# Kernel optimization log

Hardware: AMD Instinct MI355X
Metric: run time of the kernel (lower is better)

Reference implementation:

```python
import jax, jax.numpy as jnp
import numpy as np

N_QUBITS = 10
DEPTH = 5
DIM = 2 ** N_QUBITS  # 1024
NUM_CLASSES = 2
BATCH = 16384
IN_DIM = 784


def _rot_matrices(w):
    # w: [depth, n_qubits, 3] angles (phi, theta, omega); qml.Rot = RZ(omega) RY(theta) RZ(phi)
    phi, theta, omega = w[..., 0], w[..., 1], w[..., 2]
    c, s = jnp.cos(theta / 2), jnp.sin(theta / 2)
    e = lambda a: jnp.exp(1j * a.astype(jnp.complex64))
    m00 = e(-(phi + omega) / 2) * c
    m01 = -e((phi - omega) / 2) * s
    m10 = e(-(phi - omega) / 2) * s
    m11 = e((phi + omega) / 2) * c
    return jnp.stack([jnp.stack([m00, m01], -1), jnp.stack([m10, m11], -1)], -2)  # [D, n, 2, 2]


def _apply_1q(state, U, w):
    # state: [B] + [2]*n ; apply 2x2 U on qubit axis w
    s = jnp.moveaxis(state, w + 1, -1)
    s = s @ U.T
    return jnp.moveaxis(s, -1, w + 1)


def _apply_cnot(state, c, t):
    s = jnp.moveaxis(state, (c + 1, t + 1), (-2, -1))
    s = jnp.concatenate([s[..., 0:1, :], s[..., 1:2, ::-1]], axis=-2)  # flip target where control=1
    return jnp.moveaxis(s, (-2, -1), (c + 1, t + 1))


def _circuit(x, weights):
    B = x.shape[0]
    # AmplitudeEmbedding: pad_with=0, normalize=True
    amp = jnp.pad(x, ((0, 0), (0, DIM - x.shape[1])))
    amp = amp / jnp.linalg.norm(amp, axis=1, keepdims=True)
    state = amp.astype(jnp.complex64).reshape((B,) + (2,) * N_QUBITS)
    U = _rot_matrices(weights)
    for d in range(DEPTH):
        for i in range(N_QUBITS):  # entangling CNOT ring
            state = _apply_cnot(state, i, (i + 1) % N_QUBITS)
        for i in range(N_QUBITS):  # per-qubit Rot
            state = _apply_1q(state, U[d, i], i)
    probs = (state.real ** 2 + state.imag ** 2).reshape(B, DIM)
    # <Z_i> = P(bit_i = 0) - P(bit_i = 1)
    z = []
    for i in range(N_QUBITS):
        p = probs.reshape(B, 2 ** i, 2, -1)
        z.append(p[:, :, 0, :].sum((1, 2)) - p[:, :, 1, :].sum((1, 2)))
    return jnp.stack(z, axis=1)  # [B, n_qubits]


def setup_inputs() -> dict:
    key = jax.random.key(0)
    k1, k2, k3 = jax.random.split(key, 3)
    x = jax.random.normal(k1, (BATCH, IN_DIM), dtype=jnp.float32)
    weights = jax.random.uniform(k2, (DEPTH, N_QUBITS, 3), dtype=jnp.float32) * (2.0 * np.pi)
    y = jax.random.randint(k3, (BATCH,), 0, NUM_CLASSES)
    return {"x": x, "weights": weights, "y": y}


def reference(x, weights, y):
    logits = _circuit(x, weights)[:, :NUM_CLASSES]
    logp = jax.nn.log_softmax(logits, axis=-1)
    loss = -jnp.take_along_axis(logp, y[:, None], axis=1).mean()
    return loss
```

## Files before the change

### kernel.cpp

```cpp
#include <hip/hip_runtime.h>
#include <type_traits>

#define NQ 10
#define N_DEPTH 5
#define DIM 1024
#define BATCH 16384
#define IN_DIM 784
#define NGATES 50
#define KPAD 800
#define KALLOC 832
#define NT 13
#define NSLOT 768
#define NB 6

typedef float f32x2 __attribute__((ext_vector_type(2)));
typedef float f32x4 __attribute__((ext_vector_type(4)));
typedef short bf16x8 __attribute__((ext_vector_type(8)));
typedef unsigned u32x4 __attribute__((ext_vector_type(4)));

struct MaskTab {
  unsigned v[NGATES];
  unsigned p[NGATES];
  unsigned vz0, vz1;
};

constexpr MaskTab make_masks() {
  MaskTab t{};
  unsigned v[NQ], p[NQ];
  for (int i = 0; i < NQ; ++i) { v[i] = 1u << (9 - i); p[i] = 1u << (9 - i); }
  for (int d = 0; d < N_DEPTH; ++d) {
    for (int i = 0; i < NQ; ++i) {
      int c = i, tt = (i + 1) % NQ;
      v[tt] ^= v[c];
      p[c]  ^= p[tt];
    }
    for (int i = 0; i < NQ; ++i) {
      t.v[d * NQ + i] = v[i];
      t.p[d * NQ + i] = p[i];
    }
  }
  t.vz0 = v[0];
  t.vz1 = v[1];
  return t;
}

constexpr MaskTab MT = make_masks();
__constant__ MaskTab d_MT = make_masks();

struct PermTab { short slot[DIM]; };
constexpr PermTab make_perm() {
  PermTab t{};
  int a = 0, b = 256, c = 512;
  for (int m = 0; m < DIM; ++m) {
    const int p0 = __builtin_popcount((unsigned)m & MT.vz0) & 1;
    const int p1 = __builtin_popcount((unsigned)m & MT.vz1) & 1;
    if (p0 && !p1)      t.slot[m] = (short)a++;
    else if (!p0 && p1) t.slot[m] = (short)b++;
    else if (p0 && p1)  t.slot[m] = (short)c++;
    else                t.slot[m] = -1;
  }
  return t;
}
__constant__ PermTab d_PT = make_perm();

__device__ __forceinline__ f32x2 ampfma(f32x2 o, f32x2 q, f32x2 co, f32x2 cp) {
  f32x2 d;
  asm("v_pk_mul_f32 %0, %2, %1 op_sel:[0,0] op_sel_hi:[0,1]\n\t"
      "v_pk_fma_f32 %0, %2, %1, %0 op_sel:[1,1,0] op_sel_hi:[1,0,1] neg_lo:[1,0,0]\n\t"
      "v_pk_fma_f32 %0, %3, %4, %0 op_sel:[0,0,0] op_sel_hi:[0,1,1]\n\t"
      "v_pk_fma_f32 %0, %3, %4, %0 op_sel:[1,1,0] op_sel_hi:[1,0,1] neg_lo:[1,0,0]"
      : "=&v"(d)
      : "v"(o), "v"(co), "v"(cp), "v"(q));
  return d;
}

__device__ __forceinline__ float fxor(float x, unsigned m) {
  return __uint_as_float(__float_as_uint(x) ^ m);
}

__device__ __forceinline__ unsigned bf16pack(float lo, float hi) {
  unsigned a = __float_as_uint(lo), b = __float_as_uint(hi);
  unsigned ra = (a + 0x7fffu + ((a >> 16) & 1u)) >> 16;
  unsigned rb = (b + 0x7fffu + ((b >> 16) & 1u)) >> 16;
  return (ra & 0xffffu) | (rb << 16);
}

__device__ __forceinline__ unsigned cvtpk(float a, float b) {
  unsigned d;
  asm("v_cvt_pk_bf16_f32 %0, %1, %2" : "=v"(d) : "v"(a), "v"(b));
  return d;
}

__device__ __forceinline__ void gll16(const void* g, void* l) {
  __builtin_amdgcn_global_load_lds(
      (const __attribute__((address_space(1))) void*)g,
      (__attribute__((address_space(3))) void*)l, 16, 0, 0);
}

__global__ __launch_bounds__(256) void prep(const float* __restrict__ X,
                                            unsigned* __restrict__ Xb,
                                            float* __restrict__ xn2,
                                            const float* __restrict__ w,
                                            unsigned* __restrict__ W2u) {
  __shared__ f32x4 UL4[NGATES];
  __shared__ f32x2 S0[DIM];
  __shared__ f32x2 S1[DIM];

  const int tid = threadIdx.x;

  if (blockIdx.x >= 832) {
    const int row = (blockIdx.x - 832) * 8 + (tid >> 5);
    const int l32 = tid & 31;
    const float* src = X + (size_t)row * IN_DIM;
    unsigned* dst = Xb + (size_t)row * (KPAD / 2);
    float ssq = 0.0f;
    for (int c = l32; c < 100; c += 32) {
      u32x4 out;
      if (c < 98) {
        f32x4 v0 = *(const f32x4*)(src + c * 8);
        f32x4 v1 = *(const f32x4*)(src + c * 8 + 4);
        ssq += v0.x * v0.x + v0.y * v0.y + v0.z * v0.z + v0.w * v0.w +
               v1.x * v1.x + v1.y * v1.y + v1.z * v1.z + v1.w * v1.w;
        out = u32x4{cvtpk(v0.x, v0.y), cvtpk(v0.z, v0.w),
                    cvtpk(v1.x, v1.y), cvtpk(v1.z, v1.w)};
      } else {
        out = u32x4{0, 0, 0, 0};
      }
      *(u32x4*)(dst + c * 4) = out;
    }
#pragma unroll
    for (int off = 1; off < 32; off <<= 1) ssq += __shfl_xor(ssq, off);
    if (l32 == 0) xn2[row] = ssq;
    return;
  }

  if (tid < NGATES) {
    float phi = w[tid * 3 + 0], th = w[tid * 3 + 1], om = w[tid * 3 + 2];
    float ct = cosf(th * 0.5f), st = sinf(th * 0.5f);
    float aa = (phi + om) * 0.5f, bb = (phi - om) * 0.5f;
    float cA = cosf(aa), sA = sinf(aa), cB = cosf(bb), sB = sinf(bb);
    UL4[tid] = f32x4{ ct * cA, -ct * sA, -st * cB, -st * sB };
  }

  const int j = blockIdx.x;
  unsigned* rowp = W2u + (size_t)j * NSLOT;

  if (j >= IN_DIM) {
#pragma unroll
    for (int k = 0; k < 3; ++k) rowp[tid + k * 256] = 0u;
    return;
  }

#pragma unroll
  for (int k = 0; k < 4; ++k) {
    const int m = tid + k * 256;
    S0[m] = f32x2{(m == j) ? 1.0f : 0.0f, 0.0f};
  }
  __syncthreads();

  for (int g = 0; g < NGATES; ++g) {
    const f32x2* src = (g & 1) ? S1 : S0;
    f32x2* dst = (g & 1) ? S0 : S1;
    const f32x4 A = UL4[g];
    const unsigned v = d_MT.v[g];
    const unsigned p = d_MT.p[g];
#pragma unroll
    for (int k = 0; k < 4; ++k) {
      const int m = tid + k * 256;
      f32x2 o = src[m];
      f32x2 q = src[m ^ (int)p];
      const unsigned sg = (unsigned)(__popc((int)((unsigned)m & v)) & 1) << 31;
      const f32x2 co = {A.x, fxor(A.y, sg)};
      const f32x2 cp = {fxor(A.z, sg), A.w};
      dst[m] = ampfma(o, q, co, cp);
    }
    __syncthreads();
  }

  const f32x2* fin = S0;
#pragma unroll
  for (int k = 0; k < 4; ++k) {
    const int m = tid + k * 256;
    const int s = d_PT.slot[m];
    f32x2 a = fin[m];
    if (s >= 0) rowp[s] = bf16pack(a.x, a.y);
  }
}

__global__ __launch_bounds__(256) void transpose_w(const unsigned* __restrict__ W2u,
                                                   unsigned* __restrict__ W2Tu) {
  __shared__ unsigned tile[64][33];
  const int j0 = blockIdx.x * 64;
  const int n0 = blockIdx.y * 64;
  const int t = threadIdx.x;
#pragma unroll
  for (int i = 0; i < 8; ++i) {
    const int idx = i * 256 + t;
    const int jr = idx >> 5, nc = idx & 31;
    tile[jr][nc] = W2u[(size_t)(j0 + jr) * NSLOT + (n0 >> 1) + nc];
  }
  __syncthreads();
#pragma unroll
  for (int i = 0; i < 8; ++i) {
    const int idx = i * 256 + t;
    const int nr = idx >> 5, jc = idx & 31;
    const unsigned lo = tile[jc * 2][nr >> 1];
    const unsigned hi = tile[jc * 2 + 1][nr >> 1];
    const unsigned sh = (unsigned)(nr & 1) * 16u;
    const unsigned val = ((lo >> sh) & 0xffffu) | (((hi >> sh) & 0xffffu) << 16);
    W2Tu[(size_t)(n0 + nr) * (KALLOC / 2) + (j0 >> 1) + jc] = val;
  }
}

__global__ __launch_bounds__(512) void gemm_fused(const unsigned short* __restrict__ Xb,
                                                  const unsigned short* __restrict__ W2T,
                                                  float* __restrict__ accb) {
  __shared__ u32x4 lds4[8192];
  char* lds = (char*)lds4;

  const int tid = threadIdx.x;
  const int orig = blockIdx.x;
  const int bx = (orig & 7) * 48 + (orig >> 3);
  const int mb = bx / NB, nb = bx % NB;
  const int m0 = mb * 256, n0 = nb * 256;
  const int lane = tid & 63, wv = tid >> 6;
  const int wm = wv >> 2, wn = wv & 3;

  const int lrow = lane >> 3;
  const int lc = (lane & 7) ^ lrow;

  auto stage = [&](int t) {
    char* Ab = lds + (t & 1) * 65536;
    char* Bb = Ab + 32768;
    int colA = t * 64 + lc * 8;
    if (colA > 792) colA = 792;
    const int colB = t * 64 + lc * 8;
#pragma unroll
    for (int i = 0; i < 4; ++i) {
      const int g = wv * 4 + i;
      const int row = g * 8 + lrow;
      gll16(Xb + (size_t)(m0 + row) * KPAD + colA, Ab + g * 1024);
    }
#pragma unroll
    for (int i = 0; i < 4; ++i) {
      const int g = wv * 4 + i;
      const int row = g * 8 + lrow;
      gll16(W2T + (size_t)(n0 + row) * KALLOC + colB, Bb + g * 1024);
    }
  };

  stage(0);
  asm volatile("s_waitcnt vmcnt(0)" ::: "memory");
  __builtin_amdgcn_s_barrier();

  f32x4 acc[8][4];
#pragma unroll
  for (int fm = 0; fm < 8; ++fm)
#pragma unroll
    for (int fn = 0; fn < 4; ++fn) acc[fm][fn] = f32x4{0, 0, 0, 0};

  const int kc = lane >> 4;

  for (int t = 0; t < NT; ++t) {
    const char* Ab = lds + (t & 1) * 65536;
    const char* Bb = Ab + 32768;

    bf16x8 af0[8], bf0[4], af1[8], bf1[4];
#pragma unroll
    for (int f = 0; f < 8; ++f) {
      const int ar = wm * 128 + f * 16 + (lane & 15);
      af0[f] = *(const bf16x8*)(Ab + ar * 128 + ((kc ^ (ar & 7)) * 16));
    }
#pragma unroll
    for (int f = 0; f < 4; ++f) {
      const int br = wn * 64 + f * 16 + (lane & 15);
      bf0[f] = *(const bf16x8*)(Bb + br * 128 + ((kc ^ (br & 7)) * 16));
    }
    if (t < NT - 1) stage(t + 1);
#pragma unroll
    for (int f = 0; f < 8; ++f) {
      const int ar = wm * 128 + f * 16 + (lane & 15);
      af1[f] = *(const bf16x8*)(Ab + ar * 128 + (((4 + kc) ^ (ar & 7)) * 16));
    }
#pragma unroll
    for (int f = 0; f < 4; ++f) {
      const int br = wn * 64 + f * 16 + (lane & 15);
      bf1[f] = *(const bf16x8*)(Bb + br * 128 + (((4 + kc) ^ (br & 7)) * 16));
    }

    __builtin_amdgcn_s_setprio(1);
#pragma unroll
    for (int fm = 0; fm < 8; ++fm)
#pragma unroll
      for (int fn = 0; fn < 4; ++fn)
        acc[fm][fn] = __builtin_amdgcn_mfma_f32_16x16x32_bf16(
            af0[fm], bf0[fn], acc[fm][fn], 0, 0, 0);
    __builtin_amdgcn_s_setprio(0);

    __builtin_amdgcn_s_setprio(1);
#pragma unroll
    for (int fm = 0; fm < 8; ++fm)
#pragma unroll
      for (int fn = 0; fn < 4; ++fn)
        acc[fm][fn] = __builtin_amdgcn_mfma_f32_16x16x32_bf16(
            af1[fm], bf1[fn], acc[fm][fn], 0, 0, 0);
    __builtin_amdgcn_s_setprio(0);

    if (t < NT - 1) {
      asm volatile("s_waitcnt vmcnt(0)" ::: "memory");
      __builtin_amdgcn_sched_barrier(0);
      __builtin_amdgcn_s_barrier();
    }
  }

#pragma unroll
  for (int fm = 0; fm < 8; ++fm) {
    float sn[4] = {0, 0, 0, 0};
#pragma unroll
    for (int fn = 0; fn < 4; ++fn) {
#pragma unroll
      for (int r = 0; r < 4; ++r) {
        const float vv = acc[fm][fn][r];
        sn[r] = fmaf(vv, vv, sn[r]);
      }
    }
#pragma unroll
    for (int off = 1; off < 16; off <<= 1) {
#pragma unroll
      for (int r = 0; r < 4; ++r) sn[r] += __shfl_xor(sn[r], off);
    }
    if ((lane & 15) == 0) {
#pragma unroll
      for (int r = 0; r < 4; ++r) {
        const int m = m0 + wm * 128 + fm * 16 + (lane >> 4) * 4 + r;
        accb[(size_t)nb * BATCH + m] = sn[r];
      }
    }
  }
}

__global__ __launch_bounds__(256) void loss_partial(const float* __restrict__ accb,
                                                    const float* __restrict__ xn2,
                                                    const int* __restrict__ y,
                                                    float* __restrict__ partial) {
  const int s = blockIdx.x * 256 + threadIdx.x;
  const float SA = accb[0 * BATCH + s] + accb[1 * BATCH + s];
  const float SB = accb[2 * BATCH + s] + accb[3 * BATCH + s];
  const float SC = accb[4 * BATCH + s] + accb[5 * BATCH + s];
  const float n2 = xn2[s];
  const float z0 = n2 - 2.0f * (SA + SC);
  const float z1 = n2 - 2.0f * (SB + SC);
  const float inv = 1.0f / n2;
  const float l0 = z0 * inv, l1 = z1 * inv;
  const float mx = fmaxf(l0, l1);
  const float lse = mx + logf(expf(l0 - mx) + expf(l1 - mx));
  float loss = lse - ((y[s] == 0) ? l0 : l1);

  __shared__ float sm[256];
  sm[threadIdx.x] = loss;
  __syncthreads();
  for (int st = 128; st > 0; st >>= 1) {
    if (threadIdx.x < st) sm[threadIdx.x] += sm[threadIdx.x + st];
    __syncthreads();
  }
  if (threadIdx.x == 0) partial[blockIdx.x] = sm[0];
}

__global__ __launch_bounds__(64) void loss_final(const float* __restrict__ partial,
                                                 float* __restrict__ out) {
  float v = partial[threadIdx.x];
#pragma unroll
  for (int off = 1; off < 64; off <<= 1) v += __shfl_xor(v, off);
  if (threadIdx.x == 0) out[0] = v * (1.0f / (float)BATCH);
}

extern "C" void kernel_launch(void* const* d_in, const int* in_sizes, int n_in,
                              void* d_out, int out_size, void* d_ws, size_t ws_size,
                              hipStream_t stream) {
  const float* x = (const float*)d_in[0];
  const float* w = (const float*)d_in[1];
  const int*   y = (const int*)d_in[2];

  char* ws = (char*)d_ws;
  unsigned* Xb   = (unsigned*)ws;
  unsigned* W2u  = (unsigned*)(ws + 26214400);
  unsigned* W2Tu = (unsigned*)(ws + 29622272);
  float*    xn2  = (float*)(ws + 32178176);
  float*    accb = (float*)(ws + 26214400);
  float* partial = (float*)(ws + 33030144);

  prep<<<2880, 256, 0, stream>>>(x, Xb, xn2, w, W2u);
  transpose_w<<<dim3(13, 24), 256, 0, stream>>>(W2u, W2Tu);
  gemm_fused<<<384, 512, 0, stream>>>((const unsigned short*)Xb,
                                      (const unsigned short*)W2Tu, accb);
  loss_partial<<<BATCH / 256, 256, 0, stream>>>(accb, xn2, y, partial);
  loss_final<<<1, 64, 0, stream>>>(partial, (float*)d_out);
}
```

Baseline: 89.27 us.

## Switch GEMM operands from bf16 to scaled FP8 with fp8 MFMA

Quantizes the input rows and the folded circuit weight matrix to FP8 (with fixed power-of-two scales), changes the LDS staging layout, swizzle and transpose kernel for byte-wide elements, and uses the fp8 16x16x32 MFMA. The scales are undone in the loss kernel. This halves operand bytes and LDS footprint, aiming to cut memory traffic and raise matrix throughput. FP8's reduced precision risks loss accuracy, and fixed scales may saturate or underflow for other inputs.

```diff
diff --git a/kernel.cpp b/kernel.cpp
--- a/kernel.cpp
+++ b/kernel.cpp
@@ -7,7 +7,6 @@
 #define BATCH 16384
 #define IN_DIM 784
 #define NGATES 50
-#define KPAD 800
 #define KALLOC 832
 #define NT 13
 #define NSLOT 768
@@ -15,7 +14,6 @@
 
 typedef float f32x2 __attribute__((ext_vector_type(2)));
 typedef float f32x4 __attribute__((ext_vector_type(4)));
-typedef short bf16x8 __attribute__((ext_vector_type(8)));
 typedef unsigned u32x4 __attribute__((ext_vector_type(4)));
 
 struct MaskTab {
@@ -78,17 +76,10 @@
   return __uint_as_float(__float_as_uint(x) ^ m);
 }
 
-__device__ __forceinline__ unsigned bf16pack(float lo, float hi) {
-  unsigned a = __float_as_uint(lo), b = __float_as_uint(hi);
-  unsigned ra = (a + 0x7fffu + ((a >> 16) & 1u)) >> 16;
-  unsigned rb = (b + 0x7fffu + ((b >> 16) & 1u)) >> 16;
-  return (ra & 0xffffu) | (rb << 16);
-}
-
-__device__ __forceinline__ unsigned cvtpk(float a, float b) {
-  unsigned d;
-  asm("v_cvt_pk_bf16_f32 %0, %1, %2" : "=v"(d) : "v"(a), "v"(b));
-  return d;
+__device__ __forceinline__ unsigned pk4_fp8(float a, float b, float c, float d) {
+  int v = __builtin_amdgcn_cvt_pk_fp8_f32(a, b, 0, false);
+  v = __builtin_amdgcn_cvt_pk_fp8_f32(c, d, v, true);
+  return (unsigned)v;
 }
 
 __device__ __forceinline__ void gll16(const void* g, void* l) {
@@ -97,11 +88,15 @@
       (__attribute__((address_space(3))) void*)l, 16, 0, 0);
 }
 
+#define XSCALE 32.0f
+#define WSCALE 16.0f
+#define SINV   (1.0f / 262144.0f)
+
 __global__ __launch_bounds__(256) void prep(const float* __restrict__ X,
-                                            unsigned* __restrict__ Xb,
+                                            char* __restrict__ Xf8,
                                             float* __restrict__ xn2,
                                             const float* __restrict__ w,
-                                            unsigned* __restrict__ W2u) {
+                                            unsigned short* __restrict__ W2u) {
   __shared__ f32x4 UL4[NGATES];
   __shared__ f32x2 S0[DIM];
   __shared__ f32x2 S1[DIM];
@@ -112,21 +107,28 @@
     const int row = (blockIdx.x - 832) * 8 + (tid >> 5);
     const int l32 = tid & 31;
     const float* src = X + (size_t)row * IN_DIM;
-    unsigned* dst = Xb + (size_t)row * (KPAD / 2);
+    char* dst = Xf8 + (size_t)row * KALLOC;
     float ssq = 0.0f;
-    for (int c = l32; c < 100; c += 32) {
+    for (int c = l32; c < 52; c += 32) {
       u32x4 out;
-      if (c < 98) {
-        f32x4 v0 = *(const f32x4*)(src + c * 8);
-        f32x4 v1 = *(const f32x4*)(src + c * 8 + 4);
+      if (c < 49) {
+        f32x4 v0 = *(const f32x4*)(src + c * 16);
+        f32x4 v1 = *(const f32x4*)(src + c * 16 + 4);
+        f32x4 v2 = *(const f32x4*)(src + c * 16 + 8);
+        f32x4 v3 = *(const f32x4*)(src + c * 16 + 12);
         ssq += v0.x * v0.x + v0.y * v0.y + v0.z * v0.z + v0.w * v0.w +
-               v1.x * v1.x + v1.y * v1.y + v1.z * v1.z + v1.w * v1.w;
-        out = u32x4{cvtpk(v0.x, v0.y), cvtpk(v0.z, v0.w),
-                    cvtpk(v1.x, v1.y), cvtpk(v1.z, v1.w)};
+               v1.x * v1.x + v1.y * v1.y + v1.z * v1.z + v1.w * v1.w +
+               v2.x * v2.x + v2.y * v2.y + v2.z * v2.z + v2.w * v2.w +
+               v3.x * v3.x + v3.y * v3.y + v3.z * v3.z + v3.w * v3.w;
+        out = u32x4{
+          pk4_fp8(v0.x * XSCALE, v0.y * XSCALE, v0.z * XSCALE, v0.w * XSCALE),
+          pk4_fp8(v1.x * XSCALE, v1.y * XSCALE, v1.z * XSCALE, v1.w * XSCALE),
+          pk4_fp8(v2.x * XSCALE, v2.y * XSCALE, v2.z * XSCALE, v2.w * XSCALE),
+          pk4_fp8(v3.x * XSCALE, v3.y * XSCALE, v3.z * XSCALE, v3.w * XSCALE)};
       } else {
         out = u32x4{0, 0, 0, 0};
       }
-      *(u32x4*)(dst + c * 4) = out;
+      *(u32x4*)(dst + c * 16) = out;
     }
 #pragma unroll
     for (int off = 1; off < 32; off <<= 1) ssq += __shfl_xor(ssq, off);
@@ -143,11 +145,11 @@
   }
 
   const int j = blockIdx.x;
-  unsigned* rowp = W2u + (size_t)j * NSLOT;
+  unsigned short* rowp = W2u + (size_t)j * NSLOT;
 
   if (j >= IN_DIM) {
 #pragma unroll
-    for (int k = 0; k < 3; ++k) rowp[tid + k * 256] = 0u;
+    for (int k = 0; k < 3; ++k) rowp[tid + k * 256] = 0;
     return;
   }
 
@@ -183,39 +185,47 @@
     const int m = tid + k * 256;
     const int s = d_PT.slot[m];
     f32x2 a = fin[m];
-    if (s >= 0) rowp[s] = bf16pack(a.x, a.y);
-  }
-}
-
-__global__ __launch_bounds__(256) void transpose_w(const unsigned* __restrict__ W2u,
-                                                   unsigned* __restrict__ W2Tu) {
+    if (s >= 0)
+      rowp[s] = (unsigned short)(pk4_fp8(a.x * WSCALE, a.y * WSCALE,
+                                         0.0f, 0.0f) & 0xffffu);
+  }
+}
+
+__global__ __launch_bounds__(256) void transpose_w(const unsigned* __restrict__ W2u32,
+                                                   unsigned* __restrict__ W2Tu32) {
   __shared__ unsigned tile[64][33];
   const int j0 = blockIdx.x * 64;
-  const int n0 = blockIdx.y * 64;
+  const int s0 = blockIdx.y * 64;
   const int t = threadIdx.x;
 #pragma unroll
   for (int i = 0; i < 8; ++i) {
     const int idx = i * 256 + t;
-    const int jr = idx >> 5, nc = idx & 31;
-    tile[jr][nc] = W2u[(size_t)(j0 + jr) * NSLOT + (n0 >> 1) + nc];
+    const int jr = idx >> 5, sc = idx & 31;
+    tile[jr][sc] = W2u32[(size_t)(j0 + jr) * (NSLOT / 2) + (s0 >> 1) + sc];
   }
   __syncthreads();
 #pragma unroll
   for (int i = 0; i < 8; ++i) {
     const int idx = i * 256 + t;
-    const int nr = idx >> 5, jc = idx & 31;
-    const unsigned lo = tile[jc * 2][nr >> 1];
-    const unsigned hi = tile[jc * 2 + 1][nr >> 1];
-    const unsigned sh = (unsigned)(nr & 1) * 16u;
-    const unsigned val = ((lo >> sh) & 0xffffu) | (((hi >> sh) & 0xffffu) << 16);
-    W2Tu[(size_t)(n0 + nr) * (KALLOC / 2) + (j0 >> 1) + jc] = val;
-  }
-}
-
-__global__ __launch_bounds__(512) void gemm_fused(const unsigned short* __restrict__ Xb,
-                                                  const unsigned short* __restrict__ W2T,
+    const int rl = idx >> 4, jq = idx & 15;
+    const int slot = rl >> 1, c = rl & 1;
+    const int sc = slot >> 1, p = slot & 1;
+    unsigned out = 0;
+#pragma unroll
+    for (int q = 0; q < 4; ++q) {
+      const unsigned w32 = tile[jq * 4 + q][sc];
+      const unsigned h = (w32 >> (16 * p)) & 0xffffu;
+      out |= ((h >> (8 * c)) & 0xffu) << (8 * q);
+    }
+    const int orow = 2 * (s0 + slot) + c;
+    W2Tu32[((size_t)orow * KALLOC + j0 + jq * 4) >> 2] = out;
+  }
+}
+
+__global__ __launch_bounds__(512) void gemm_fused(const char* __restrict__ Xf8,
+                                                  const char* __restrict__ W2T,
                                                   float* __restrict__ accb) {
-  __shared__ u32x4 lds4[8192];
+  __shared__ u32x4 lds4[4096];
   char* lds = (char*)lds4;
 
   const int tid = threadIdx.x;
@@ -226,26 +236,24 @@
   const int lane = tid & 63, wv = tid >> 6;
   const int wm = wv >> 2, wn = wv & 3;
 
-  const int lrow = lane >> 3;
-  const int lc = (lane & 7) ^ lrow;
+  const int rl = lane >> 2;
+  const int csrc = (lane & 3) ^ (rl & 3) ^ ((rl >> 2) & 3);
 
   auto stage = [&](int t) {
-    char* Ab = lds + (t & 1) * 65536;
-    char* Bb = Ab + 32768;
-    int colA = t * 64 + lc * 8;
-    if (colA > 792) colA = 792;
-    const int colB = t * 64 + lc * 8;
-#pragma unroll
-    for (int i = 0; i < 4; ++i) {
-      const int g = wv * 4 + i;
-      const int row = g * 8 + lrow;
-      gll16(Xb + (size_t)(m0 + row) * KPAD + colA, Ab + g * 1024);
-    }
-#pragma unroll
-    for (int i = 0; i < 4; ++i) {
-      const int g = wv * 4 + i;
-      const int row = g * 8 + lrow;
-      gll16(W2T + (size_t)(n0 + row) * KALLOC + colB, Bb + g * 1024);
+    char* Ab = lds + (t & 1) * 32768;
+    char* Bb = Ab + 16384;
+    const int col = t * 64 + csrc * 16;
+#pragma unroll
+    for (int i = 0; i < 2; ++i) {
+      const int g = wv * 2 + i;
+      const int row = g * 16 + rl;
+      gll16(Xf8 + (size_t)(m0 + row) * KALLOC + col, Ab + g * 1024);
+    }
+#pragma unroll
+    for (int i = 0; i < 2; ++i) {
+      const int g = wv * 2 + i;
+      const int row = g * 16 + rl;
+      gll16(W2T + (size_t)(n0 + row) * KALLOC + col, Bb + g * 1024);
     }
   };
 
@@ -262,30 +270,36 @@
   const int kc = lane >> 4;
 
   for (int t = 0; t < NT; ++t) {
-    const char* Ab = lds + (t & 1) * 65536;
-    const char* Bb = Ab + 32768;
-
-    bf16x8 af0[8], bf0[4], af1[8], bf1[4];
+    const char* Ab = lds + (t & 1) * 32768;
+    const char* Bb = Ab + 16384;
+
+    long af0[8], bf0[4], af1[8], bf1[4];
 #pragma unroll
     for (int f = 0; f < 8; ++f) {
       const int ar = wm * 128 + f * 16 + (lane & 15);
-      af0[f] = *(const bf16x8*)(Ab + ar * 128 + ((kc ^ (ar & 7)) * 16));
+      const int sw = (ar & 3) ^ ((ar >> 2) & 3);
+      af0[f] = *(const long*)(Ab + ar * 64 + (((kc >> 1) ^ sw) * 16) + (kc & 1) * 8);
     }
 #pragma unroll
     for (int f = 0; f < 4; ++f) {
       const int br = wn * 64 + f * 16 + (lane & 15);
-      bf0[f] = *(const bf16x8*)(Bb + br * 128 + ((kc ^ (br & 7)) * 16));
+      const int sw = (br & 3) ^ ((br >> 2) & 3);
+      bf0[f] = *(const long*)(Bb + br * 64 + (((kc >> 1) ^ sw) * 16) + (kc & 1) * 8);
     }
     if (t < NT - 1) stage(t + 1);
 #pragma unroll
     for (int f = 0; f < 8; ++f) {
       const int ar = wm * 128 + f * 16 + (lane & 15);
-      af1[f] = *(const bf16x8*)(Ab + ar * 128 + (((4 + kc) ^ (ar & 7)) * 16));
+      const int sw = (ar & 3) ^ ((ar >> 2) & 3);
+      const int kb = 4 + kc;
+      af1[f] = *(const long*)(Ab + ar * 64 + (((kb >> 1) ^ sw) * 16) + (kb & 1) * 8);
     }
 #pragma unroll
     for (int f = 0; f < 4; ++f) {
       const int br = wn * 64 + f * 16 + (lane & 15);
-      bf1[f] = *(const bf16x8*)(Bb + br * 128 + (((4 + kc) ^ (br & 7)) * 16));
+      const int sw = (br & 3) ^ ((br >> 2) & 3);
+      const int kb = 4 + kc;
+      bf1[f] = *(const long*)(Bb + br * 64 + (((kb >> 1) ^ sw) * 16) + (kb & 1) * 8);
     }
 
     __builtin_amdgcn_s_setprio(1);
@@ -293,7 +307,7 @@
     for (int fm = 0; fm < 8; ++fm)
 #pragma unroll
       for (int fn = 0; fn < 4; ++fn)
-        acc[fm][fn] = __builtin_amdgcn_mfma_f32_16x16x32_bf16(
+        acc[fm][fn] = __builtin_amdgcn_mfma_f32_16x16x32_fp8_fp8(
             af0[fm], bf0[fn], acc[fm][fn], 0, 0, 0);
     __builtin_amdgcn_s_setprio(0);
 
@@ -302,7 +316,7 @@
     for (int fm = 0; fm < 8; ++fm)
 #pragma unroll
       for (int fn = 0; fn < 4; ++fn)
-        acc[fm][fn] = __builtin_amdgcn_mfma_f32_16x16x32_bf16(
+        acc[fm][fn] = __builtin_amdgcn_mfma_f32_16x16x32_fp8_fp8(
             af1[fm], bf1[fn], acc[fm][fn], 0, 0, 0);
     __builtin_amdgcn_s_setprio(0);
 
@@ -344,9 +358,9 @@
                                                     const int* __restrict__ y,
                                                     float* __restrict__ partial) {
   const int s = blockIdx.x * 256 + threadIdx.x;
-  const float SA = accb[0 * BATCH + s] + accb[1 * BATCH + s];
-  const float SB = accb[2 * BATCH + s] + accb[3 * BATCH + s];
-  const float SC = accb[4 * BATCH + s] + accb[5 * BATCH + s];
+  const float SA = (accb[0 * BATCH + s] + accb[1 * BATCH + s]) * SINV;
+  const float SB = (accb[2 * BATCH + s] + accb[3 * BATCH + s]) * SINV;
+  const float SC = (accb[4 * BATCH + s] + accb[5 * BATCH + s]) * SINV;
   const float n2 = xn2[s];
   const float z0 = n2 - 2.0f * (SA + SC);
   const float z1 = n2 - 2.0f * (SB + SC);
@@ -382,17 +396,17 @@
   const int*   y = (const int*)d_in[2];
 
   char* ws = (char*)d_ws;
-  unsigned* Xb   = (unsigned*)ws;
-  unsigned* W2u  = (unsigned*)(ws + 26214400);
-  unsigned* W2Tu = (unsigned*)(ws + 29622272);
-  float*    xn2  = (float*)(ws + 32178176);
-  float*    accb = (float*)(ws + 26214400);
-  float* partial = (float*)(ws + 33030144);
-
-  prep<<<2880, 256, 0, stream>>>(x, Xb, xn2, w, W2u);
-  transpose_w<<<dim3(13, 24), 256, 0, stream>>>(W2u, W2Tu);
-  gemm_fused<<<384, 512, 0, stream>>>((const unsigned short*)Xb,
-                                      (const unsigned short*)W2Tu, accb);
+  char*     Xf8  = ws;
+  unsigned short* W2u = (unsigned short*)(ws + 13631488);
+  char*     W2Tu = ws + 14909440;
+  float*    xn2  = (float*)(ws + 16187392);
+  float*    accb = (float*)(ws + 16252928);
+  float* partial = (float*)(ws + 16646144);
+
+  prep<<<2880, 256, 0, stream>>>(x, Xf8, xn2, w, W2u);
+  transpose_w<<<dim3(13, 12), 256, 0, stream>>>((const unsigned*)W2u,
+                                                (unsigned*)W2Tu);
+  gemm_fused<<<384, 512, 0, stream>>>(Xf8, W2Tu, accb);
   loss_partial<<<BATCH / 256, 256, 0, stream>>>(accb, xn2, y, partial);
   loss_final<<<1, 64, 0, stream>>>(partial, (float*)d_out);
 }
```

Result: faster. 87.42 us (-2.1%).
